# Kernel optimization log

Hardware: AMD Instinct MI355X
Metric: run time of the kernel (lower is better)

The kernel has to match this reference:

```python
import jax, jax.numpy as jnp
import numpy as np

B, H, W, C = 8, 128, 128, 384
WS, SHIFT, NH = 8, 4, 12
N = WS * WS            # tokens per window = 64
HD = C // NH           # head dim = 32
SCALE = HD ** -0.5


def _rel_pos_index():
    ch, cw = np.meshgrid(np.arange(WS), np.arange(WS), indexing='ij')
    cf = np.stack([ch.ravel(), cw.ravel()])            # (2, N)
    rel = cf[:, :, None] - cf[:, None, :]              # (2, N, N)
    rel = rel.transpose(1, 2, 0)                       # (N, N, 2)
    rel[:, :, 0] += WS - 1
    rel[:, :, 1] += WS - 1
    rel[:, :, 0] *= 2 * WS - 1
    return jnp.asarray(rel.sum(-1))                    # (N, N) int

REL_IDX = _rel_pos_index()


def _shift_mask():
    # standard Swin SW-MSA mask, built once with numpy
    img = np.zeros((1, H, W, 1), np.float32)
    cnt = 0
    for hs in (slice(0, -WS), slice(-WS, -SHIFT), slice(-SHIFT, None)):
        for ws_ in (slice(0, -WS), slice(-WS, -SHIFT), slice(-SHIFT, None)):
            img[:, hs, ws_, :] = cnt
            cnt += 1
    m = img.reshape(1, H // WS, WS, W // WS, WS, 1).transpose(0, 1, 3, 2, 4, 5)
    m = m.reshape(-1, N)                               # (nW, N)
    am = m[:, None, :] - m[:, :, None]                 # (nW, N, N)
    return np.where(am != 0, np.float32(-100.0), np.float32(0.0))


def _ln(x, g, b, eps=1e-5):
    mu = x.mean(-1, keepdims=True)
    var = ((x - mu) ** 2).mean(-1, keepdims=True)
    return (x - mu) * jax.lax.rsqrt(var + eps) * g + b


def setup_inputs() -> dict:
    key = jax.random.key(0)
    ks = jax.random.split(key, 10)
    s = 0.02
    return {
        'x': jax.random.normal(ks[0], (B, H * W, C), jnp.float32),
        'qkv_w': jax.random.normal(ks[1], (3 * C, C), jnp.float32) * s,
        'qkv_b': jnp.zeros((3 * C,), jnp.float32),
        'proj_w': jax.random.normal(ks[2], (C, C), jnp.float32) * s,
        'proj_b': jnp.zeros((C,), jnp.float32),
        'rel_bias_table': jax.random.normal(ks[3], ((2 * WS - 1) ** 2, NH), jnp.float32) * s,
        'g1': jnp.ones((C,), jnp.float32), 'b1': jnp.zeros((C,), jnp.float32),
        'g2': jnp.ones((C,), jnp.float32), 'b2': jnp.zeros((C,), jnp.float32),
        'fc1_w': jax.random.normal(ks[4], (4 * C, C), jnp.float32) * s,
        'fc1_b': jnp.zeros((4 * C,), jnp.float32),
        'fc2_w': jax.random.normal(ks[5], (C, 4 * C), jnp.float32) * s,
        'fc2_b': jnp.zeros((C,), jnp.float32),
        'attn_mask': jnp.asarray(_shift_mask()),       # (nW, N, N)
    }


def reference(x, qkv_w, qkv_b, proj_w, proj_b, rel_bias_table, g1, b1, g2, b2,
              fc1_w, fc1_b, fc2_w, fc2_b, attn_mask):
    shortcut = x
    h = _ln(x, g1, b1).reshape(B, H, W, C)
    # cyclic shift (SW-MSA)
    h = jnp.roll(h, (-SHIFT, -SHIFT), axis=(1, 2))
    # window partition -> (B*nW, N, C)
    nWh, nWw = H // WS, W // WS
    hw = h.reshape(B, nWh, WS, nWw, WS, C).transpose(0, 1, 3, 2, 4, 5)
    hw = hw.reshape(B * nWh * nWw, N, C)
    # qkv projection
    qkv = jnp.einsum('bnc,dc->bnd', hw, qkv_w) + qkv_b   # (Bw, N, 3C)
    qkv = qkv.reshape(-1, N, 3, NH, HD).transpose(2, 0, 3, 1, 4)
    q, k, v = qkv[0], qkv[1], qkv[2]                    # (Bw, NH, N, HD)
    attn = jnp.einsum('bhnd,bhmd->bhnm', q * SCALE, k)  # (Bw, NH, N, N)
    bias = rel_bias_table[REL_IDX.reshape(-1)].reshape(N, N, NH)
    attn = attn + bias.transpose(2, 0, 1)[None]
    # shift mask: attn viewed as (B, nW, NH, N, N) + mask (nW, 1, N, N)
    nW = nWh * nWw
    attn = attn.reshape(B, nW, NH, N, N) + attn_mask[None, :, None]
    attn = jax.nn.softmax(attn.reshape(-1, NH, N, N), axis=-1)
    out = jnp.einsum('bhnm,bhmd->bnhd', attn, v).reshape(-1, N, C)
    out = jnp.einsum('bnc,dc->bnd', out, proj_w) + proj_b
    # window reverse + un-shift
    out = out.reshape(B, nWh, nWw, WS, WS, C).transpose(0, 1, 3, 2, 4, 5)
    out = out.reshape(B, H, W, C)
    out = jnp.roll(out, (SHIFT, SHIFT), axis=(1, 2)).reshape(B, H * W, C)
    x = shortcut + out
    # MLP block
    h2 = _ln(x, g2, b2)
    h2 = jax.nn.gelu(jnp.einsum('blc,dc->bld', h2, fc1_w) + fc1_b, approximate=False)
    h2 = jnp.einsum('bld,cd->blc', h2, fc2_w) + fc2_b
    return x + h2
```

## Files before the change

kernel.cpp:

```cpp
#include <hip/hip_runtime.h>
#include <hip/hip_bf16.h>
#include <math.h>

typedef __attribute__((ext_vector_type(4))) float f32x4;
typedef __attribute__((ext_vector_type(8))) short bf16x8;

__device__ __forceinline__ unsigned short f2bf(float f) {
  unsigned int x = __builtin_bit_cast(unsigned int, f);
  x += 0x7fffu + ((x >> 16) & 1u);
  return (unsigned short)(x >> 16);
}
__device__ __forceinline__ float bf2f(unsigned short u) {
  unsigned int x = ((unsigned int)u) << 16;
  return __builtin_bit_cast(float, x);
}

__device__ __forceinline__ void gload_lds16(const void* g, void* l) {
  __builtin_amdgcn_global_load_lds(
      (const __attribute__((address_space(1))) unsigned int*)g,
      (__attribute__((address_space(3))) unsigned int*)l, 16, 0, 0);
}

__global__ void cvt_f32_bf16(const float* __restrict__ s, unsigned short* __restrict__ d, int n) {
  int i = blockIdx.x * 256 + threadIdx.x;
  if (i < n) d[i] = f2bf(s[i]);
}

template <int REMAP>
__global__ __launch_bounds__(256)
void ln_kernel(const float* __restrict__ x, const float* __restrict__ g,
               const float* __restrict__ b, unsigned short* __restrict__ dst_o) {
  int r = blockIdx.x * 4 + (threadIdx.x >> 6);
  int lane = threadIdx.x & 63;
  size_t src;
  if (REMAP) {
    int w = r >> 6, t = r & 63;
    int bb = w >> 8, wi = (w >> 4) & 15, wj = w & 15;
    int i = t >> 3, j = t & 7;
    int p = (wi * 8 + i + 4) & 127, q = (wj * 8 + j + 4) & 127;
    src = ((size_t)bb * 16384 + p * 128 + q) * 384;
  } else {
    src = (size_t)r * 384;
  }
  float v[6];
  float s = 0.f, s2 = 0.f;
#pragma unroll
  for (int m = 0; m < 6; ++m) {
    v[m] = x[src + lane + 64 * m];
    s += v[m];
    s2 += v[m] * v[m];
  }
#pragma unroll
  for (int o2 = 1; o2 < 64; o2 <<= 1) {
    s += __shfl_xor(s, o2);
    s2 += __shfl_xor(s2, o2);
  }
  float mu = s * (1.f / 384.f);
  float var = s2 * (1.f / 384.f) - mu * mu;
  float ri = rsqrtf(var + 1e-5f);
  size_t dst = (size_t)r * 384;
#pragma unroll
  for (int m = 0; m < 6; ++m) {
    int c = lane + 64 * m;
    dst_o[dst + c] = f2bf((v[m] - mu) * ri * g[c] + b[c]);
  }
}

__global__ __launch_bounds__(256)
void ln_bf16(const unsigned short* __restrict__ x, const float* __restrict__ g,
             const float* __restrict__ b, unsigned short* __restrict__ dst_o) {
  int r = blockIdx.x * 4 + (threadIdx.x >> 6);
  int lane = threadIdx.x & 63;
  size_t src = (size_t)r * 384;
  float v[6];
  float s = 0.f, s2 = 0.f;
#pragma unroll
  for (int m = 0; m < 3; ++m) {
    unsigned int u = *(const unsigned int*)&x[src + lane * 2 + 128 * m];
    v[2 * m] = bf2f((unsigned short)(u & 0xffffu));
    v[2 * m + 1] = bf2f((unsigned short)(u >> 16));
    s += v[2 * m] + v[2 * m + 1];
    s2 += v[2 * m] * v[2 * m] + v[2 * m + 1] * v[2 * m + 1];
  }
#pragma unroll
  for (int o2 = 1; o2 < 64; o2 <<= 1) {
    s += __shfl_xor(s, o2);
    s2 += __shfl_xor(s2, o2);
  }
  float mu = s * (1.f / 384.f);
  float var = s2 * (1.f / 384.f) - mu * mu;
  float ri = rsqrtf(var + 1e-5f);
#pragma unroll
  for (int m = 0; m < 3; ++m) {
    int c = lane * 2 + 128 * m;
    unsigned int lo = f2bf((v[2 * m] - mu) * ri * g[c] + b[c]);
    unsigned int hi = f2bf((v[2 * m + 1] - mu) * ri * g[c + 1] + b[c + 1]);
    *(unsigned int*)&dst_o[src + c] = lo | (hi << 16);
  }
}

template <int EPI>
__global__ __launch_bounds__(512, 1)
void gemm8(const unsigned short* __restrict__ A, const unsigned short* __restrict__ Bw,
           const float* __restrict__ bias, int M, int N, int K, int NT,
           unsigned short* __restrict__ Obf, const void* __restrict__ resid,
           float* __restrict__ Of) {
  extern __shared__ unsigned short lds[];
  const int tid = threadIdx.x;
  const int lane = tid & 63;
  const int wid = tid >> 6;
  const int wm = wid >> 1, wn = wid & 1;
  const int li = lane & 15, lg = lane >> 4;

  const int nwg = gridDim.x;
  const int orig = blockIdx.x;
  const int q = nwg >> 3, r = nwg & 7;
  const int xcd = orig & 7, loc = orig >> 3;
  const int wg = (xcd < r ? xcd * (q + 1) : r * (q + 1) + (xcd - r) * q) + loc;
  const int m0 = (wg / NT) * 256;
  const int n0 = (wg % NT) * 128;

  const int srow = wid * 8 + (lane >> 3);
  const int scol = ((lane & 7) ^ (lane >> 3)) * 8;
  const unsigned short* gA = A + (size_t)(m0 + srow) * K + scol;
  const unsigned short* gB = Bw + (size_t)(n0 + srow) * K + scol;

  const int nk = K >> 6;
  const int fswz = (li & 7) << 3;
  f32x4 acc[4][4] = {};

  auto stage = [&](int k, int b) {
    unsigned short* dA = lds + b * 24576;
    unsigned short* dB = dA + 16384;
#pragma unroll
    for (int c = 0; c < 4; ++c)
      gload_lds16(gA + (size_t)(c * 64) * K + k * 64, &dA[c * 4096 + wid * 512]);
#pragma unroll
    for (int c = 0; c < 2; ++c)
      gload_lds16(gB + (size_t)(c * 64) * K + k * 64, &dB[c * 4096 + wid * 512]);
  };

  stage(0, 0);
  stage(1, 1);

  int cur = 0;
  for (int t = 0; t < nk; ++t) {
    if (t < nk - 1) {
      asm volatile("s_waitcnt vmcnt(6)" ::: "memory");
    } else {
      asm volatile("s_waitcnt vmcnt(0)" ::: "memory");
    }
    __builtin_amdgcn_s_barrier();
    __builtin_amdgcn_sched_barrier(0);
    if (t + 2 < nk) {
      int nb = cur + 2;
      if (nb >= 3) nb -= 3;
      stage(t + 2, nb);
    }
    const unsigned short* pA = lds + cur * 24576;
    const unsigned short* pB = pA + 16384;
#pragma unroll
    for (int kk = 0; kk < 2; ++kk) {
      bf16x8 a[4], bb[4];
#pragma unroll
      for (int f = 0; f < 4; ++f) {
        a[f] = *(const bf16x8*)&pA[(wm * 64 + f * 16 + li) * 64 + ((kk * 32 + lg * 8) ^ fswz)];
        bb[f] = *(const bf16x8*)&pB[(wn * 64 + f * 16 + li) * 64 + ((kk * 32 + lg * 8) ^ fswz)];
      }
      __builtin_amdgcn_s_setprio(1);
#pragma unroll
      for (int mf = 0; mf < 4; ++mf)
#pragma unroll
        for (int nf = 0; nf < 4; ++nf)
          acc[mf][nf] = __builtin_amdgcn_mfma_f32_16x16x32_bf16(a[mf], bb[nf], acc[mf][nf], 0, 0, 0);
      __builtin_amdgcn_s_setprio(0);
    }
    ++cur;
    if (cur == 3) cur = 0;
  }

#pragma unroll
  for (int mf = 0; mf < 4; ++mf) {
#pragma unroll
    for (int r2 = 0; r2 < 4; ++r2) {
      int mrow = m0 + wm * 64 + mf * 16 + lg * 4 + r2;
      size_t orow = (size_t)mrow;
      if (EPI == 2) {
        int w = mrow >> 6, t = mrow & 63;
        int bb2 = w >> 8, wi = (w >> 4) & 15, wj = w & 15;
        int i = t >> 3, j = t & 7;
        int p = (wi * 8 + i + 4) & 127, qq = (wj * 8 + j + 4) & 127;
        orow = (size_t)bb2 * 16384 + p * 128 + qq;
      }
#pragma unroll
      for (int nf = 0; nf < 4; ++nf) {
        int col = n0 + wn * 64 + nf * 16 + li;
        float v = acc[mf][nf][r2] + bias[col];
        if (EPI == 0) {
          Obf[(size_t)mrow * N + col] = f2bf(v);
        } else if (EPI == 1) {
          float y = 1.5957691f * (v + 0.044715f * v * v * v);
          float gl = v * __builtin_amdgcn_rcpf(1.f + __expf(-y));
          Obf[(size_t)mrow * N + col] = f2bf(gl);
        } else if (EPI == 2) {
          const float* rx = (const float*)resid;
          Obf[orow * 384 + col] = f2bf(v + rx[orow * 384 + col]);
        } else {
          const unsigned short* rx = (const unsigned short*)resid;
          Of[(size_t)mrow * N + col] = v + bf2f(rx[(size_t)mrow * N + col]);
        }
      }
    }
  }
}

__global__ __launch_bounds__(256, 2)
void attn_kernel(const unsigned short* __restrict__ qkv, const float* __restrict__ btab,
                 const float* __restrict__ mask, unsigned short* __restrict__ out) {
  __shared__ unsigned short v_lds[4][64 * 40];
  __shared__ unsigned short p_lds[4][64 * 72];
  const int w = blockIdx.x;
  const int tid = threadIdx.x;
  const int wid = tid >> 6, lane = tid & 63;
  const int li = lane & 15, lg = lane >> 4;
  const float* mrow = mask + (size_t)(w & 255) * 4096;
  const size_t base = (size_t)w * 64;
  const float SC = 0.17677669529663688f;

#pragma unroll 1
  for (int hi = 0; hi < 3; ++hi) {
    int h = wid * 3 + hi;
    bf16x8 aq[4], bk[4];
#pragma unroll
    for (int f = 0; f < 4; ++f) {
      size_t off = (base + f * 16 + li) * 1152 + h * 32 + lg * 8;
      aq[f] = *(const bf16x8*)&qkv[off];
      bk[f] = *(const bf16x8*)&qkv[off + 384];
    }
    f32x4 s[4][4] = {};
#pragma unroll
    for (int mf = 0; mf < 4; ++mf)
#pragma unroll
      for (int nf = 0; nf < 4; ++nf)
        s[mf][nf] = __builtin_amdgcn_mfma_f32_16x16x32_bf16(aq[mf], bk[nf], s[mf][nf], 0, 0, 0);

    {
      const unsigned short* vp = &qkv[(base + lane) * 1152 + 768 + h * 32];
      unsigned short* dp = &v_lds[wid][lane * 40];
#pragma unroll
      for (int c = 0; c < 4; ++c) *(bf16x8*)&dp[c * 8] = *(const bf16x8*)&vp[c * 8];
    }

#pragma unroll
    for (int mf = 0; mf < 4; ++mf) {
#pragma unroll
      for (int r = 0; r < 4; ++r) {
        int m = mf * 16 + lg * 4 + r;
        float mx = -1e30f;
#pragma unroll
        for (int nf = 0; nf < 4; ++nf) {
          int n = nf * 16 + li;
          int ridx = ((m >> 3) - (n >> 3) + 7) * 15 + (m & 7) - (n & 7) + 7;
          float val = s[mf][nf][r] * SC + btab[ridx * 12 + h] + mrow[m * 64 + n];
          s[mf][nf][r] = val;
          mx = fmaxf(mx, val);
        }
#pragma unroll
        for (int o2 = 1; o2 < 16; o2 <<= 1) mx = fmaxf(mx, __shfl_xor(mx, o2));
        float sum = 0.f;
#pragma unroll
        for (int nf = 0; nf < 4; ++nf) {
          float e = __expf(s[mf][nf][r] - mx);
          s[mf][nf][r] = e;
          sum += e;
        }
#pragma unroll
        for (int o2 = 1; o2 < 16; o2 <<= 1) sum += __shfl_xor(sum, o2);
        float inv = __builtin_amdgcn_rcpf(sum);
#pragma unroll
        for (int nf = 0; nf < 4; ++nf) s[mf][nf][r] *= inv;
      }
    }

#pragma unroll
    for (int mf = 0; mf < 4; ++mf)
#pragma unroll
      for (int nf = 0; nf < 4; ++nf)
#pragma unroll
        for (int r = 0; r < 4; ++r) {
          int m = mf * 16 + lg * 4 + r, n = nf * 16 + li;
          p_lds[wid][m * 72 + n] = f2bf(s[mf][nf][r]);
        }

    f32x4 o[4][2] = {};
#pragma unroll
    for (int kf = 0; kf < 2; ++kf) {
      bf16x8 bv[2];
#pragma unroll
      for (int df = 0; df < 2; ++df) {
        bf16x8 t;
#pragma unroll
        for (int e = 0; e < 8; ++e)
          t[e] = (short)v_lds[wid][(kf * 32 + lg * 8 + e) * 40 + df * 16 + li];
        bv[df] = t;
      }
#pragma unroll
      for (int mf = 0; mf < 4; ++mf) {
        bf16x8 pa = *(const bf16x8*)&p_lds[wid][(mf * 16 + li) * 72 + kf * 32 + lg * 8];
#pragma unroll
        for (int df = 0; df < 2; ++df)
          o[mf][df] = __builtin_amdgcn_mfma_f32_16x16x32_bf16(pa, bv[df], o[mf][df], 0, 0, 0);
      }
    }

#pragma unroll
    for (int mf = 0; mf < 4; ++mf)
#pragma unroll
      for (int df = 0; df < 2; ++df)
#pragma unroll
        for (int r = 0; r < 4; ++r) {
          size_t row = base + mf * 16 + lg * 4 + r;
          out[row * 384 + h * 32 + df * 16 + li] = f2bf(o[mf][df][r]);
        }
  }
}

extern "C" void kernel_launch(void* const* d_in, const int* in_sizes, int n_in,
                              void* d_out, int out_size, void* d_ws, size_t ws_size,
                              hipStream_t stream) {
  const float* x      = (const float*)d_in[0];
  const float* qkv_w  = (const float*)d_in[1];
  const float* qkv_b  = (const float*)d_in[2];
  const float* proj_w = (const float*)d_in[3];
  const float* proj_b = (const float*)d_in[4];
  const float* rel    = (const float*)d_in[5];
  const float* g1     = (const float*)d_in[6];
  const float* b1     = (const float*)d_in[7];
  const float* g2     = (const float*)d_in[8];
  const float* b2     = (const float*)d_in[9];
  const float* fc1_w  = (const float*)d_in[10];
  const float* fc1_b  = (const float*)d_in[11];
  const float* fc2_w  = (const float*)d_in[12];
  const float* fc2_b  = (const float*)d_in[13];
  const float* mask   = (const float*)d_in[14];
  float* out = (float*)d_out;
  char* ws = (char*)d_ws;

  const int M = 131072;
  const int LDS_BYTES = 3 * 49152;
  (void)hipFuncSetAttribute((const void*)gemm8<0>, hipFuncAttributeMaxDynamicSharedMemorySize, LDS_BYTES);
  (void)hipFuncSetAttribute((const void*)gemm8<1>, hipFuncAttributeMaxDynamicSharedMemorySize, LDS_BYTES);
  (void)hipFuncSetAttribute((const void*)gemm8<2>, hipFuncAttributeMaxDynamicSharedMemorySize, LDS_BYTES);
  (void)hipFuncSetAttribute((const void*)gemm8<3>, hipFuncAttributeMaxDynamicSharedMemorySize, LDS_BYTES);

  unsigned short* hw     = (unsigned short*)ws;
  unsigned short* qkv    = (unsigned short*)(ws + 100663296);
  unsigned short* hmid   = (unsigned short*)ws;
  unsigned short* attn_o = (unsigned short*)(ws + 402653184);
  unsigned short* ln2o   = attn_o;
  unsigned short* x1b    = (unsigned short*)(ws + 503316480);
  unsigned short* wq     = (unsigned short*)(ws + 603979776);
  unsigned short* wp     = wq + 442368;
  unsigned short* w1     = wp + 147456;
  unsigned short* w2     = w1 + 589824;

  cvt_f32_bf16<<<(442368 + 255) / 256, 256, 0, stream>>>(qkv_w, wq, 442368);
  cvt_f32_bf16<<<(147456 + 255) / 256, 256, 0, stream>>>(proj_w, wp, 147456);
  cvt_f32_bf16<<<(589824 + 255) / 256, 256, 0, stream>>>(fc1_w, w1, 589824);
  cvt_f32_bf16<<<(589824 + 255) / 256, 256, 0, stream>>>(fc2_w, w2, 589824);

  ln_kernel<1><<<M / 4, 256, 0, stream>>>(x, g1, b1, hw);

  gemm8<0><<<512 * 9, 512, LDS_BYTES, stream>>>(hw, wq, qkv_b, M, 1152, 384, 9, qkv, nullptr, nullptr);

  attn_kernel<<<2048, 256, 0, stream>>>(qkv, rel, mask, attn_o);

  gemm8<2><<<512 * 3, 512, LDS_BYTES, stream>>>(attn_o, wp, proj_b, M, 384, 384, 3, x1b, x, nullptr);

  ln_bf16<<<M / 4, 256, 0, stream>>>(x1b, g2, b2, ln2o);

  gemm8<1><<<512 * 12, 512, LDS_BYTES, stream>>>(ln2o, w1, fc1_b, M, 1536, 384, 12, hmid, nullptr, nullptr);

  gemm8<3><<<512 * 3, 512, LDS_BYTES, stream>>>(hmid, w2, fc2_b, M, 384, 1536, 3, nullptr, x1b, out);
}
```

Measured before the change: 1.145 ms.

## Widen GEMM N-tile to 192 with double buffering, split attention heads across grid

The GEMM tile grows from 256x128 to 256x192, with 6 N-fragments per wave. This raises arithmetic intensity and cuts the number of workgroups and the reloads of the A tile. The 3-stage LDS ring becomes a 2-buffer ping-pong scheme that waits on vmcnt(0) and adds extra barriers per k-step, which may expose load latency. The attention kernel moves its head loop onto a second grid dimension to gain parallelism, and the four weight-conversion launches are merged into one kernel.

```diff
diff --git a/kernel.cpp b/kernel.cpp
--- a/kernel.cpp
+++ b/kernel.cpp
@@ -21,9 +21,18 @@
       (__attribute__((address_space(3))) unsigned int*)l, 16, 0, 0);
 }
 
-__global__ void cvt_f32_bf16(const float* __restrict__ s, unsigned short* __restrict__ d, int n) {
+__global__ void cvt_all(const float* __restrict__ s0, int n0, const float* __restrict__ s1, int n1,
+                        const float* __restrict__ s2, int n2, const float* __restrict__ s3, int n3,
+                        unsigned short* __restrict__ d) {
   int i = blockIdx.x * 256 + threadIdx.x;
-  if (i < n) d[i] = f2bf(s[i]);
+  if (i >= n0 + n1 + n2 + n3) return;
+  const float* s;
+  int off;
+  if (i < n0) { s = s0; off = 0; }
+  else if (i < n0 + n1) { s = s1; off = n0; }
+  else if (i < n0 + n1 + n2) { s = s2; off = n0 + n1; }
+  else { s = s3; off = n0 + n1 + n2; }
+  d[i] = f2bf(s[i - off]);
 }
 
 template <int REMAP>
@@ -101,7 +110,7 @@
 
 template <int EPI>
 __global__ __launch_bounds__(512, 1)
-void gemm8(const unsigned short* __restrict__ A, const unsigned short* __restrict__ Bw,
+void gemm9(const unsigned short* __restrict__ A, const unsigned short* __restrict__ Bw,
            const float* __restrict__ bias, int M, int N, int K, int NT,
            unsigned short* __restrict__ Obf, const void* __restrict__ resid,
            float* __restrict__ Of) {
@@ -118,7 +127,7 @@
   const int xcd = orig & 7, loc = orig >> 3;
   const int wg = (xcd < r ? xcd * (q + 1) : r * (q + 1) + (xcd - r) * q) + loc;
   const int m0 = (wg / NT) * 256;
-  const int n0 = (wg % NT) * 128;
+  const int n0 = (wg % NT) * 192;
 
   const int srow = wid * 8 + (lane >> 3);
   const int scol = ((lane & 7) ^ (lane >> 3)) * 8;
@@ -127,56 +136,55 @@
 
   const int nk = K >> 6;
   const int fswz = (li & 7) << 3;
-  f32x4 acc[4][4] = {};
-
-  auto stage = [&](int k, int b) {
-    unsigned short* dA = lds + b * 24576;
-    unsigned short* dB = dA + 16384;
+  f32x4 acc[4][6] = {};
+
+  auto stage = [&](int k, unsigned short* dst) {
+    unsigned short* dB = dst + 16384;
 #pragma unroll
     for (int c = 0; c < 4; ++c)
-      gload_lds16(gA + (size_t)(c * 64) * K + k * 64, &dA[c * 4096 + wid * 512]);
-#pragma unroll
-    for (int c = 0; c < 2; ++c)
+      gload_lds16(gA + (size_t)(c * 64) * K + k * 64, &dst[c * 4096 + wid * 512]);
+#pragma unroll
+    for (int c = 0; c < 3; ++c)
       gload_lds16(gB + (size_t)(c * 64) * K + k * 64, &dB[c * 4096 + wid * 512]);
   };
 
-  stage(0, 0);
-  stage(1, 1);
-
-  int cur = 0;
-  for (int t = 0; t < nk; ++t) {
-    if (t < nk - 1) {
-      asm volatile("s_waitcnt vmcnt(6)" ::: "memory");
-    } else {
-      asm volatile("s_waitcnt vmcnt(0)" ::: "memory");
-    }
+  unsigned short* const buf0 = lds;
+  unsigned short* const buf1 = lds + 28672;
+
+  auto tile = [&](int t, unsigned short* cur, unsigned short* nxt) {
+    if (t + 1 < nk) stage(t + 1, nxt);
+    const unsigned short* pA = cur;
+    const unsigned short* pB = cur + 16384;
+#pragma unroll
+    for (int kk = 0; kk < 2; ++kk) {
+      bf16x8 a[4], b[6];
+#pragma unroll
+      for (int f = 0; f < 4; ++f)
+        a[f] = *(const bf16x8*)&pA[(wm * 64 + f * 16 + li) * 64 + ((kk * 32 + lg * 8) ^ fswz)];
+#pragma unroll
+      for (int f = 0; f < 6; ++f)
+        b[f] = *(const bf16x8*)&pB[(wn * 96 + f * 16 + li) * 64 + ((kk * 32 + lg * 8) ^ fswz)];
+      __builtin_amdgcn_s_barrier();
+      __builtin_amdgcn_s_setprio(1);
+#pragma unroll
+      for (int mf = 0; mf < 4; ++mf)
+#pragma unroll
+        for (int nf = 0; nf < 6; ++nf)
+          acc[mf][nf] = __builtin_amdgcn_mfma_f32_16x16x32_bf16(a[mf], b[nf], acc[mf][nf], 0, 0, 0);
+      __builtin_amdgcn_s_setprio(0);
+      if (kk == 0) __builtin_amdgcn_s_barrier();
+    }
+    asm volatile("s_waitcnt vmcnt(0)" ::: "memory");
     __builtin_amdgcn_s_barrier();
-    __builtin_amdgcn_sched_barrier(0);
-    if (t + 2 < nk) {
-      int nb = cur + 2;
-      if (nb >= 3) nb -= 3;
-      stage(t + 2, nb);
-    }
-    const unsigned short* pA = lds + cur * 24576;
-    const unsigned short* pB = pA + 16384;
-#pragma unroll
-    for (int kk = 0; kk < 2; ++kk) {
-      bf16x8 a[4], bb[4];
-#pragma unroll
-      for (int f = 0; f < 4; ++f) {
-        a[f] = *(const bf16x8*)&pA[(wm * 64 + f * 16 + li) * 64 + ((kk * 32 + lg * 8) ^ fswz)];
-        bb[f] = *(const bf16x8*)&pB[(wn * 64 + f * 16 + li) * 64 + ((kk * 32 + lg * 8) ^ fswz)];
-      }
-      __builtin_amdgcn_s_setprio(1);
-#pragma unroll
-      for (int mf = 0; mf < 4; ++mf)
-#pragma unroll
-        for (int nf = 0; nf < 4; ++nf)
-          acc[mf][nf] = __builtin_amdgcn_mfma_f32_16x16x32_bf16(a[mf], bb[nf], acc[mf][nf], 0, 0, 0);
-      __builtin_amdgcn_s_setprio(0);
-    }
-    ++cur;
-    if (cur == 3) cur = 0;
+  };
+
+  stage(0, buf0);
+  asm volatile("s_waitcnt vmcnt(0)" ::: "memory");
+  __builtin_amdgcn_s_barrier();
+
+  for (int t = 0; t < nk; t += 2) {
+    tile(t, buf0, buf1);
+    tile(t + 1, buf1, buf0);
   }
 
 #pragma unroll
@@ -193,8 +201,8 @@
         orow = (size_t)bb2 * 16384 + p * 128 + qq;
       }
 #pragma unroll
-      for (int nf = 0; nf < 4; ++nf) {
-        int col = n0 + wn * 64 + nf * 16 + li;
+      for (int nf = 0; nf < 6; ++nf) {
+        int col = n0 + wn * 96 + nf * 16 + li;
         float v = acc[mf][nf][r2] + bias[col];
         if (EPI == 0) {
           Obf[(size_t)mrow * N + col] = f2bf(v);
@@ -220,6 +228,7 @@
   __shared__ unsigned short v_lds[4][64 * 40];
   __shared__ unsigned short p_lds[4][64 * 72];
   const int w = blockIdx.x;
+  const int hi = blockIdx.y;
   const int tid = threadIdx.x;
   const int wid = tid >> 6, lane = tid & 63;
   const int li = lane & 15, lg = lane >> 4;
@@ -227,102 +236,99 @@
   const size_t base = (size_t)w * 64;
   const float SC = 0.17677669529663688f;
 
-#pragma unroll 1
-  for (int hi = 0; hi < 3; ++hi) {
-    int h = wid * 3 + hi;
-    bf16x8 aq[4], bk[4];
-#pragma unroll
-    for (int f = 0; f < 4; ++f) {
-      size_t off = (base + f * 16 + li) * 1152 + h * 32 + lg * 8;
-      aq[f] = *(const bf16x8*)&qkv[off];
-      bk[f] = *(const bf16x8*)&qkv[off + 384];
-    }
-    f32x4 s[4][4] = {};
-#pragma unroll
-    for (int mf = 0; mf < 4; ++mf)
-#pragma unroll
-      for (int nf = 0; nf < 4; ++nf)
-        s[mf][nf] = __builtin_amdgcn_mfma_f32_16x16x32_bf16(aq[mf], bk[nf], s[mf][nf], 0, 0, 0);
-
-    {
-      const unsigned short* vp = &qkv[(base + lane) * 1152 + 768 + h * 32];
-      unsigned short* dp = &v_lds[wid][lane * 40];
-#pragma unroll
-      for (int c = 0; c < 4; ++c) *(bf16x8*)&dp[c * 8] = *(const bf16x8*)&vp[c * 8];
-    }
-
+  int h = wid * 3 + hi;
+  bf16x8 aq[4], bk[4];
+#pragma unroll
+  for (int f = 0; f < 4; ++f) {
+    size_t off = (base + f * 16 + li) * 1152 + h * 32 + lg * 8;
+    aq[f] = *(const bf16x8*)&qkv[off];
+    bk[f] = *(const bf16x8*)&qkv[off + 384];
+  }
+  f32x4 s[4][4] = {};
+#pragma unroll
+  for (int mf = 0; mf < 4; ++mf)
+#pragma unroll
+    for (int nf = 0; nf < 4; ++nf)
+      s[mf][nf] = __builtin_amdgcn_mfma_f32_16x16x32_bf16(aq[mf], bk[nf], s[mf][nf], 0, 0, 0);
+
+  {
+    const unsigned short* vp = &qkv[(base + lane) * 1152 + 768 + h * 32];
+    unsigned short* dp = &v_lds[wid][lane * 40];
+#pragma unroll
+    for (int c = 0; c < 4; ++c) *(bf16x8*)&dp[c * 8] = *(const bf16x8*)&vp[c * 8];
+  }
+
+#pragma unroll
+  for (int mf = 0; mf < 4; ++mf) {
+#pragma unroll
+    for (int r = 0; r < 4; ++r) {
+      int m = mf * 16 + lg * 4 + r;
+      float mx = -1e30f;
+#pragma unroll
+      for (int nf = 0; nf < 4; ++nf) {
+        int n = nf * 16 + li;
+        int ridx = ((m >> 3) - (n >> 3) + 7) * 15 + (m & 7) - (n & 7) + 7;
+        float val = s[mf][nf][r] * SC + btab[ridx * 12 + h] + mrow[m * 64 + n];
+        s[mf][nf][r] = val;
+        mx = fmaxf(mx, val);
+      }
+#pragma unroll
+      for (int o2 = 1; o2 < 16; o2 <<= 1) mx = fmaxf(mx, __shfl_xor(mx, o2));
+      float sum = 0.f;
+#pragma unroll
+      for (int nf = 0; nf < 4; ++nf) {
+        float e = __expf(s[mf][nf][r] - mx);
+        s[mf][nf][r] = e;
+        sum += e;
+      }
+#pragma unroll
+      for (int o2 = 1; o2 < 16; o2 <<= 1) sum += __shfl_xor(sum, o2);
+      float inv = __builtin_amdgcn_rcpf(sum);
+#pragma unroll
+      for (int nf = 0; nf < 4; ++nf) s[mf][nf][r] *= inv;
+    }
+  }
+
+#pragma unroll
+  for (int mf = 0; mf < 4; ++mf)
+#pragma unroll
+    for (int nf = 0; nf < 4; ++nf)
+#pragma unroll
+      for (int r = 0; r < 4; ++r) {
+        int m = mf * 16 + lg * 4 + r, n = nf * 16 + li;
+        p_lds[wid][m * 72 + n] = f2bf(s[mf][nf][r]);
+      }
+
+  f32x4 o[4][2] = {};
+#pragma unroll
+  for (int kf = 0; kf < 2; ++kf) {
+    bf16x8 bv[2];
+#pragma unroll
+    for (int df = 0; df < 2; ++df) {
+      bf16x8 t;
+#pragma unroll
+      for (int e = 0; e < 8; ++e)
+        t[e] = (short)v_lds[wid][(kf * 32 + lg * 8 + e) * 40 + df * 16 + li];
+      bv[df] = t;
+    }
 #pragma unroll
     for (int mf = 0; mf < 4; ++mf) {
+      bf16x8 pa = *(const bf16x8*)&p_lds[wid][(mf * 16 + li) * 72 + kf * 32 + lg * 8];
+#pragma unroll
+      for (int df = 0; df < 2; ++df)
+        o[mf][df] = __builtin_amdgcn_mfma_f32_16x16x32_bf16(pa, bv[df], o[mf][df], 0, 0, 0);
+    }
+  }
+
+#pragma unroll
+  for (int mf = 0; mf < 4; ++mf)
+#pragma unroll
+    for (int df = 0; df < 2; ++df)
 #pragma unroll
       for (int r = 0; r < 4; ++r) {
-        int m = mf * 16 + lg * 4 + r;
-        float mx = -1e30f;
-#pragma unroll
-        for (int nf = 0; nf < 4; ++nf) {
-          int n = nf * 16 + li;
-          int ridx = ((m >> 3) - (n >> 3) + 7) * 15 + (m & 7) - (n & 7) + 7;
-          float val = s[mf][nf][r] * SC + btab[ridx * 12 + h] + mrow[m * 64 + n];
-          s[mf][nf][r] = val;
-          mx = fmaxf(mx, val);
-        }
-#pragma unroll
-        for (int o2 = 1; o2 < 16; o2 <<= 1) mx = fmaxf(mx, __shfl_xor(mx, o2));
-        float sum = 0.f;
-#pragma unroll
-        for (int nf = 0; nf < 4; ++nf) {
-          float e = __expf(s[mf][nf][r] - mx);
-          s[mf][nf][r] = e;
-          sum += e;
-        }
-#pragma unroll
-        for (int o2 = 1; o2 < 16; o2 <<= 1) sum += __shfl_xor(sum, o2);
-        float inv = __builtin_amdgcn_rcpf(sum);
-#pragma unroll
-        for (int nf = 0; nf < 4; ++nf) s[mf][nf][r] *= inv;
-      }
-    }
-
-#pragma unroll
-    for (int mf = 0; mf < 4; ++mf)
-#pragma unroll
-      for (int nf = 0; nf < 4; ++nf)
-#pragma unroll
-        for (int r = 0; r < 4; ++r) {
-          int m = mf * 16 + lg * 4 + r, n = nf * 16 + li;
-          p_lds[wid][m * 72 + n] = f2bf(s[mf][nf][r]);
-        }
-
-    f32x4 o[4][2] = {};
-#pragma unroll
-    for (int kf = 0; kf < 2; ++kf) {
-      bf16x8 bv[2];
-#pragma unroll
-      for (int df = 0; df < 2; ++df) {
-        bf16x8 t;
-#pragma unroll
-        for (int e = 0; e < 8; ++e)
-          t[e] = (short)v_lds[wid][(kf * 32 + lg * 8 + e) * 40 + df * 16 + li];
-        bv[df] = t;
-      }
-#pragma unroll
-      for (int mf = 0; mf < 4; ++mf) {
-        bf16x8 pa = *(const bf16x8*)&p_lds[wid][(mf * 16 + li) * 72 + kf * 32 + lg * 8];
-#pragma unroll
-        for (int df = 0; df < 2; ++df)
-          o[mf][df] = __builtin_amdgcn_mfma_f32_16x16x32_bf16(pa, bv[df], o[mf][df], 0, 0, 0);
-      }
-    }
-
-#pragma unroll
-    for (int mf = 0; mf < 4; ++mf)
-#pragma unroll
-      for (int df = 0; df < 2; ++df)
-#pragma unroll
-        for (int r = 0; r < 4; ++r) {
-          size_t row = base + mf * 16 + lg * 4 + r;
-          out[row * 384 + h * 32 + df * 16 + li] = f2bf(o[mf][df][r]);
-        }
-  }
+        size_t row = base + mf * 16 + lg * 4 + r;
+        out[row * 384 + h * 32 + df * 16 + li] = f2bf(o[mf][df][r]);
+      }
 }
 
 extern "C" void kernel_launch(void* const* d_in, const int* in_sizes, int n_in,
@@ -347,11 +353,11 @@
   char* ws = (char*)d_ws;
 
   const int M = 131072;
-  const int LDS_BYTES = 3 * 49152;
-  (void)hipFuncSetAttribute((const void*)gemm8<0>, hipFuncAttributeMaxDynamicSharedMemorySize, LDS_BYTES);
-  (void)hipFuncSetAttribute((const void*)gemm8<1>, hipFuncAttributeMaxDynamicSharedMemorySize, LDS_BYTES);
-  (void)hipFuncSetAttribute((const void*)gemm8<2>, hipFuncAttributeMaxDynamicSharedMemorySize, LDS_BYTES);
-  (void)hipFuncSetAttribute((const void*)gemm8<3>, hipFuncAttributeMaxDynamicSharedMemorySize, LDS_BYTES);
+  const int LDS_BYTES = 2 * 57344;
+  (void)hipFuncSetAttribute((const void*)gemm9<0>, hipFuncAttributeMaxDynamicSharedMemorySize, LDS_BYTES);
+  (void)hipFuncSetAttribute((const void*)gemm9<1>, hipFuncAttributeMaxDynamicSharedMemorySize, LDS_BYTES);
+  (void)hipFuncSetAttribute((const void*)gemm9<2>, hipFuncAttributeMaxDynamicSharedMemorySize, LDS_BYTES);
+  (void)hipFuncSetAttribute((const void*)gemm9<3>, hipFuncAttributeMaxDynamicSharedMemorySize, LDS_BYTES);
 
   unsigned short* hw     = (unsigned short*)ws;
   unsigned short* qkv    = (unsigned short*)(ws + 100663296);
@@ -364,22 +370,20 @@
   unsigned short* w1     = wp + 147456;
   unsigned short* w2     = w1 + 589824;
 
-  cvt_f32_bf16<<<(442368 + 255) / 256, 256, 0, stream>>>(qkv_w, wq, 442368);
-  cvt_f32_bf16<<<(147456 + 255) / 256, 256, 0, stream>>>(proj_w, wp, 147456);
-  cvt_f32_bf16<<<(589824 + 255) / 256, 256, 0, stream>>>(fc1_w, w1, 589824);
-  cvt_f32_bf16<<<(589824 + 255) / 256, 256, 0, stream>>>(fc2_w, w2, 589824);
+  cvt_all<<<(442368 + 147456 + 589824 + 589824 + 255) / 256, 256, 0, stream>>>(
+      qkv_w, 442368, proj_w, 147456, fc1_w, 589824, fc2_w, 589824, wq);
 
   ln_kernel<1><<<M / 4, 256, 0, stream>>>(x, g1, b1, hw);
 
-  gemm8<0><<<512 * 9, 512, LDS_BYTES, stream>>>(hw, wq, qkv_b, M, 1152, 384, 9, qkv, nullptr, nullptr);
-
-  attn_kernel<<<2048, 256, 0, stream>>>(qkv, rel, mask, attn_o);
-
-  gemm8<2><<<512 * 3, 512, LDS_BYTES, stream>>>(attn_o, wp, proj_b, M, 384, 384, 3, x1b, x, nullptr);
+  gemm9<0><<<512 * 6, 512, LDS_BYTES, stream>>>(hw, wq, qkv_b, M, 1152, 384, 6, qkv, nullptr, nullptr);
+
+  attn_kernel<<<dim3(2048, 3), 256, 0, stream>>>(qkv, rel, mask, attn_o);
+
+  gemm9<2><<<512 * 2, 512, LDS_BYTES, stream>>>(attn_o, wp, proj_b, M, 384, 384, 2, x1b, x, nullptr);
 
   ln_bf16<<<M / 4, 256, 0, stream>>>(x1b, g2, b2, ln2o);
 
-  gemm8<1><<<512 * 12, 512, LDS_BYTES, stream>>>(ln2o, w1, fc1_b, M, 1536, 384, 12, hmid, nullptr, nullptr);
-
-  gemm8<3><<<512 * 3, 512, LDS_BYTES, stream>>>(hmid, w2, fc2_b, M, 384, 1536, 3, nullptr, x1b, out);
-}
+  gemm9<1><<<512 * 8, 512, LDS_BYTES, stream>>>(ln2o, w1, fc1_b, M, 1536, 384, 8, hmid, nullptr, nullptr);
+
+  gemm9<3><<<512 * 2, 512, LDS_BYTES, stream>>>(hmid, w2, fc2_b, M, 384, 1536, 2, nullptr, x1b, out);
+}
```

New measurement: 1.147 ms. No clear change (+0.1%).
